# Kernel optimization log

Hardware: AMD Instinct MI355X
Metric: run time of the kernel (lower is better)

The kernel has to match this reference:

```python
import jax, jax.numpy as jnp
from jax import lax
import numpy as np

SAMPLE_RATIO = 0.25
K = 20          # nsample from group_args
SLOPE = 0.2     # leakyrelu negative_slope
EPS = 1e-5      # BatchNorm eps


def fps(p, m):
    """Furthest point sampling. p: [B,N,3] -> idx [B,m] int32."""
    B, N, _ = p.shape

    def step(carry, _):
        dist, last_idx = carry                      # [B,N], [B]
        last_pt = jnp.take_along_axis(p, last_idx[:, None, None], axis=1)  # [B,1,3]
        d = jnp.sum((p - last_pt) ** 2, axis=-1)    # [B,N]
        dist = jnp.minimum(dist, d)
        nxt = jnp.argmax(dist, axis=1).astype(jnp.int32)
        return (dist, nxt), last_idx

    dist0 = jnp.full((B, N), 1e10, dtype=p.dtype)
    idx0 = jnp.zeros((B,), dtype=jnp.int32)
    _, idxs = lax.scan(step, (dist0, idx0), None, length=m)
    return jnp.transpose(idxs)                      # [B,m]


def knn_idx(q, p, k):
    """q: [B,M,3] queries, p: [B,N,3] -> [B,M,k] indices of k nearest."""
    # squared distances, [B,M,N] (the memory-bound intermediate)
    d = (jnp.sum(q * q, -1)[:, :, None]
         + jnp.sum(p * p, -1)[:, None, :]
         - 2.0 * jnp.einsum('bmd,bnd->bmn', q, p))
    _, idx = lax.top_k(-d, k)
    return idx


def convblock(x, W, g, b):
    """1x1 Conv2d (bias=False) -> leakyrelu(0.2) -> BatchNorm2d (train-mode)."""
    x = jnp.einsum('oc,bcmk->bomk', W, x)
    x = jnp.where(x >= 0, x, SLOPE * x)
    mean = jnp.mean(x, axis=(0, 2, 3), keepdims=True)
    var = jnp.var(x, axis=(0, 2, 3), keepdims=True)
    return g[None, :, None, None] * (x - mean) * lax.rsqrt(var + EPS) + b[None, :, None, None]


def setup_inputs() -> dict:
    key = jax.random.key(0)
    ks = jax.random.split(key, 4)
    C = 64
    p = jax.random.normal(ks[0], (4, 8192, 3), dtype=jnp.float32)
    # kaiming-normal-ish conv weights (1x1 kernels flattened to [out,in])
    W1 = jax.random.normal(ks[1], (C, 6), dtype=jnp.float32) * np.sqrt(2.0 / 6)
    W2 = jax.random.normal(ks[2], (C, C), dtype=jnp.float32) * np.sqrt(2.0 / C)
    W3 = jax.random.normal(ks[3], (C, C), dtype=jnp.float32) * np.sqrt(2.0 / C)
    ones = jnp.ones((C,), jnp.float32)
    zeros = jnp.zeros((C,), jnp.float32)
    return {"p": p, "W1": W1, "g1": ones, "b1": zeros,
            "W2": W2, "g2": ones, "b2": zeros,
            "W3": W3, "g3": ones, "b3": zeros}


def reference(p, W1, g1, b1, W2, g2, b2, W3, g3, b3):
    B, N, _ = p.shape
    M = int(N * SAMPLE_RATIO)
    # features default to xyz: f = p^T, [B,3,N]; we keep [B,N,3] layout for gathers
    idx = fps(p, M)                                              # [B,M]
    p1 = jnp.take_along_axis(p, idx[:, :, None], axis=1)         # [B,M,3]
    nidx = knn_idx(p1, p, K)                                     # [B,M,K]
    batch = jnp.arange(B)[:, None, None]
    grouped = p[batch, nidx]                                     # [B,M,K,3] gathered xyz (== gathered features)
    dp = grouped - p1[:, :, None, :]                             # [B,M,K,3] relative coords
    # cat((dp, gf), dim=1) in channel-first layout -> [B,6,M,K]
    gf = jnp.concatenate([dp, grouped], axis=-1)                 # [B,M,K,6]
    x = jnp.transpose(gf, (0, 3, 1, 2))                          # [B,6,M,K]
    x = convblock(x, W1, g1, b1)
    x = convblock(x, W2, g2, b2)
    x = convblock(x, W3, g3, b3)
    return jnp.max(x, axis=-1)                                   # [B,64,M]
```

## Files before the change

### kernel.cpp

```cpp
#include <hip/hip_runtime.h>
#include <cstdint>
#include <cstddef>


#define B_ 4
#define N_ 8192
#define M_ 2048
#define K_ 20
#define BMK (B_*M_*K_)
#define EPS_ 1e-5f
#define TILE_ 1024
#define PERS 248

typedef unsigned long long ull;
typedef float f32x2 __attribute__((ext_vector_type(2)));

__device__ __forceinline__ ull packkey(float d, int idx) {
  unsigned int bb = __float_as_uint(d);
  bb ^= (bb & 0x80000000u) ? 0xFFFFFFFFu : 0x80000000u;
  return ((ull)bb << 32) | (unsigned int)idx;
}
__device__ __forceinline__ float keymaxf(ull k) {
  unsigned int hb = (unsigned int)(k >> 32);
  unsigned int fb = (hb & 0x80000000u) ? (hb ^ 0x80000000u) : ~hb;
  return __uint_as_float(fb);
}
__device__ __forceinline__ void insert20(ull* keys, ull key) {
#pragma unroll
  for (int i = 19; i > 0; --i) {
    ull lo = keys[i-1];
    keys[i] = (key < lo) ? lo : ((key < keys[i]) ? key : keys[i]);
  }
  keys[0] = (key < keys[0]) ? key : keys[0];
}

#define DPPMAXU(V, CTRL) {                                                           \
    unsigned int nh = (unsigned int)__builtin_amdgcn_update_dpp(                     \
        (int)V, (int)V, CTRL, 0xF, 0xF, false);                                      \
    V = (nh > V) ? nh : V; }

__global__ __launch_bounds__(512)
void fpsknn_kernel(const float* __restrict__ p, float* __restrict__ p1,
                   float* __restrict__ gfp, const float* __restrict__ W1,
                   float* __restrict__ stats, int* __restrict__ prog) {
  __shared__ union {
    struct { float4 pts4[N_]; unsigned int slotsv[2][8]; int idxsel[2]; } f;
    struct { float4 tile[TILE_]; ull mk[8*32*20]; float bs[128]; } k;
  } sm;
  const int tid = threadIdx.x;

  if (blockIdx.x < B_) {
#pragma clang fp contract(off)
    const int b = blockIdx.x;
    const float* pb = p + (size_t)b * (N_*3);
    float* p1b = p1 + (size_t)b * (M_*3);
    float4* pts4 = sm.f.pts4;
    const int wv = tid >> 6;
    const int base = tid * 16;
    f32x2 X[8], Y[8], Z[8], D[8];
#pragma unroll
    for (int j = 0; j < 8; ++j) {
      int i = base + 2*j;
      float x0 = pb[i*3+0], y0 = pb[i*3+1], z0 = pb[i*3+2];
      float x1 = pb[i*3+3], y1 = pb[i*3+4], z1 = pb[i*3+5];
      X[j] = (f32x2){x0, x1};
      Y[j] = (f32x2){y0, y1};
      Z[j] = (f32x2){z0, z1};
      D[j] = (f32x2){1e10f, 1e10f};
      pts4[i]   = make_float4(x0, y0, z0, 0.f);
      pts4[i+1] = make_float4(x1, y1, z1, 0.f);
    }
    if (tid < 2) sm.f.idxsel[tid] = 0x7FFFFFFF;
    float qx = pb[0], qy = pb[1], qz = pb[2];
    if (tid == 0) { p1b[0] = qx; p1b[1] = qy; p1b[2] = qz; }
    __syncthreads();
    for (int t = 1; t < M_; ++t) {
      const int cur = t & 1;
      f32x2 q2x = (f32x2){qx, qx};
      f32x2 q2y = (f32x2){qy, qy};
      f32x2 q2z = (f32x2){qz, qz};
      f32x2 tmx = (f32x2){-1.f, -1.f};
#pragma unroll
      for (int j = 0; j < 8; ++j) {
        f32x2 dx = X[j] - q2x;
        f32x2 dy = Y[j] - q2y;
        f32x2 dz = Z[j] - q2z;
        f32x2 s = (dx*dx + dy*dy) + dz*dz;
        f32x2 dj = __builtin_elementwise_min(D[j], s);
        D[j] = dj;
        tmx = __builtin_elementwise_max(tmx, dj);
      }
      float tm = fmaxf(tmx.x, tmx.y);
      const unsigned int tmb = __float_as_uint(tm);
      unsigned int hv = tmb;
      DPPMAXU(hv, 0x111)
      DPPMAXU(hv, 0x112)
      DPPMAXU(hv, 0x114)
      DPPMAXU(hv, 0x118)
      DPPMAXU(hv, 0x142)
      DPPMAXU(hv, 0x143)
      if ((tid & 63) == 63) sm.f.slotsv[cur][wv] = hv;
      __syncthreads();
      if (tid == 0) sm.f.idxsel[cur ^ 1] = 0x7FFFFFFF;
      unsigned int g = sm.f.slotsv[cur][0];
#pragma unroll
      for (int j = 1; j < 8; ++j) { unsigned int s2 = sm.f.slotsv[cur][j]; g = (s2 > g) ? s2 : g; }
      if (tmb == g) {
        int fj = 0x7FFFFFFF;
#pragma unroll
        for (int j = 7; j >= 0; --j) {
          if (__float_as_uint(D[j].y) == g) fj = base + 2*j + 1;
          if (__float_as_uint(D[j].x) == g) fj = base + 2*j;
        }
        atomicMin(&sm.f.idxsel[cur], fj);
      }
      __syncthreads();
      int sel = sm.f.idxsel[cur];
      sel = __builtin_amdgcn_readfirstlane(sel);
      float4 qv = pts4[sel];
      qx = qv.x; qy = qv.y; qz = qv.z;
      if (tid == 0) {
        p1b[t*3+0] = qx; p1b[t*3+1] = qy; p1b[t*3+2] = qz;
        if ((t & 63) == 63)
          __hip_atomic_store(&prog[b], t, __ATOMIC_RELEASE, __HIP_MEMORY_SCOPE_AGENT);
      }
    }
    if (tid == 0)
      __hip_atomic_store(&prog[b], M_, __ATOMIC_RELEASE, __HIP_MEMORY_SCOPE_AGENT);
    return;
  }

  float4* tile = sm.k.tile;
  ull* mk = sm.k.mk;
  float* gfl = (float*)sm.k.tile;
  float* bs = sm.k.bs;
  for (int ord = (int)blockIdx.x - B_; ord < 1024; ord += PERS) {
    const int b = ord & 3;
    const int q0 = (ord >> 2) * 8;
    if (tid == 0) {
      while (__hip_atomic_load(&prog[b], __ATOMIC_ACQUIRE, __HIP_MEMORY_SCOPE_AGENT) < q0 + 7)
        __builtin_amdgcn_s_sleep(16);
    }
    __syncthreads();
    { int pv = __hip_atomic_load(&prog[b], __ATOMIC_ACQUIRE, __HIP_MEMORY_SCOPE_AGENT);
      asm volatile("" :: "v"(pv)); }

    const int ql = (tid >> 5) & 7;
    const int part = tid & 31;
    const int m = q0 + ql;
    const float* pb = p + (size_t)b*(N_*3);
    const float* qp_ = p1 + ((size_t)b*M_ + m)*3;
    float qx = qp_[0], qy = qp_[1], qz = qp_[2];
    float qq = __fadd_rn(__fadd_rn(__fmul_rn(qx,qx), __fmul_rn(qy,qy)), __fmul_rn(qz,qz));
    ull keys[20];
#pragma unroll
    for (int i = 0; i < 20; ++i) keys[i] = 0xFF8000007FFFFFFFull;
    float maxf = __uint_as_float(0x7F800000u);
    for (int t0 = 0; t0 < N_; t0 += TILE_) {
      __syncthreads();
      for (int i = tid; i < TILE_; i += 512) {
        float x = pb[(t0+i)*3+0], y = pb[(t0+i)*3+1], z = pb[(t0+i)*3+2];
        float pp = __fadd_rn(__fadd_rn(__fmul_rn(x,x), __fmul_rn(y,y)), __fmul_rn(z,z));
        tile[i] = make_float4(x, y, z, pp);
      }
      __syncthreads();
      if (tid < 256) {
        const int sbase = part * 32;
        for (int s = 0; s < 32; ++s) {
          int ss = sbase + ((s + part) & 31);
          float4 pt = tile[ss];
          float qp = fmaf(pt.z, qz, fmaf(pt.y, qy, __fmul_rn(pt.x, qx)));
          float d = __fsub_rn(__fadd_rn(qq, pt.w), __fmul_rn(2.0f, qp));
          if (d <= maxf) {
            ull key = packkey(d, t0 + ss);
            if (key < keys[19]) { insert20(keys, key); maxf = keymaxf(keys[19]); }
          }
        }
      }
    }
    if (tid < 256) {
      ull* myslot = &mk[(ql*32 + part)*20];
#pragma unroll
      for (int i = 0; i < 20; ++i) myslot[i] = keys[i];
    }
    __syncthreads();
    if (tid < 256 && part == 0) {
      for (int pp2 = 1; pp2 < 32; ++pp2) {
        const ull* os = &mk[(ql*32 + pp2)*20];
        for (int i = 0; i < 20; ++i) {
          ull k = os[i];
          if (k >= keys[19]) break;
          insert20(keys, k);
        }
      }
      ull* myslot = &mk[(ql*32)*20];
#pragma unroll
      for (int i = 0; i < 20; ++i) myslot[i] = keys[i];
    }
    __syncthreads();
    for (int w = tid; w < 8*K_; w += 512) {
      int ql2 = w / K_;
      int kk = w - ql2*K_;
      ull key = mk[ql2*32*20 + kk];
      int idx = (int)(unsigned int)(key & 0xFFFFFFFFu);
      float gx = pb[idx*3+0], gy = pb[idx*3+1], gz = pb[idx*3+2];
      int m2 = q0 + ql2;
      const float* qv = p1 + ((size_t)b*M_ + m2)*3;
      size_t col = ((size_t)(b*M_ + m2))*K_ + kk;
      float d0 = __fsub_rn(gx, qv[0]);
      float d1 = __fsub_rn(gy, qv[1]);
      float d2 = __fsub_rn(gz, qv[2]);
      gfp[0*BMK + col] = d0;
      gfp[1*BMK + col] = d1;
      gfp[2*BMK + col] = d2;
      gfp[3*BMK + col] = gx;
      gfp[4*BMK + col] = gy;
      gfp[5*BMK + col] = gz;
      gfl[w*6+0] = d0; gfl[w*6+1] = d1; gfl[w*6+2] = d2;
      gfl[w*6+3] = gx; gfl[w*6+4] = gy; gfl[w*6+5] = gz;
    }
    __syncthreads();
    {
      const int lane = tid & 63;
      const int grp = tid >> 6;
      float w1r[6];
#pragma unroll
      for (int c = 0; c < 6; ++c) w1r[c] = W1[lane*6 + c];
      float acc = 0.f, accq = 0.f;
      for (int cc = 0; cc < 20; ++cc) {
        const float* gv = &gfl[(grp*20 + cc)*6];
        float y = __fmul_rn(w1r[0], gv[0]);
#pragma unroll
        for (int c = 1; c < 6; ++c) y = fmaf(w1r[c], gv[c], y);
        float u = (y >= 0.f) ? y : 0.2f*y;
        acc += u;
        accq = fmaf(u, u, accq);
      }
      if (tid < 128) bs[tid] = 0.f;
      __syncthreads();
      atomicAdd(&bs[lane], acc);
      atomicAdd(&bs[64+lane], accq);
      __syncthreads();
      if (tid < 128) atomicAdd(&stats[tid], bs[tid]);
    }
  }
}

__device__ __forceinline__ void bn_coeff(const float* __restrict__ st,
                                         const float* __restrict__ g,
                                         const float* __restrict__ bb,
                                         int o, float& A, float& C) {
  const float inv = 1.0f / (float)BMK;
  float mean = st[o] * inv;
  float var  = st[64+o] * inv - mean*mean;
  float a = g[o] / sqrtf(var + EPS_);
  A = a;
  C = fmaf(-a, mean, bb[o]);
}

__device__ __forceinline__ void gridbar(int* c, int expected) {
  __syncthreads();
  if (threadIdx.x == 0) {
    __hip_atomic_fetch_add(c, 1, __ATOMIC_ACQ_REL, __HIP_MEMORY_SCOPE_AGENT);
    while (__hip_atomic_load(c, __ATOMIC_ACQUIRE, __HIP_MEMORY_SCOPE_AGENT) < expected)
      __builtin_amdgcn_s_sleep(2);
  }
  __syncthreads();
}

__global__ __launch_bounds__(256)
void tail_kernel(const float* __restrict__ gfp, const float* __restrict__ W1,
                 float* __restrict__ stats,
                 const float* __restrict__ g1, const float* __restrict__ b1,
                 const float* __restrict__ W2, float* __restrict__ u2t,
                 const float* __restrict__ W3,
                 const float* __restrict__ g2, const float* __restrict__ b2,
                 const float* __restrict__ g3, const float* __restrict__ b3,
                 float* __restrict__ out, int* __restrict__ bar,
                 float* __restrict__ pmx, float* __restrict__ pmn) {
  const int tid = threadIdx.x;
  const int nblk = (int)gridDim.x;
  const int lane = tid & 63;
  const int wid = ((int)blockIdx.x*256 + tid) >> 6;
  const int nw = (nblk*256) >> 6;
  __shared__ float sA[64], sC[64];
  __shared__ float bs[128];
  __shared__ float xbuf[4][64];
  float* xb = xbuf[(tid >> 6) & 3];

  {
    if (tid < 64) bn_coeff(stats, g1, b1, tid, sA[tid], sC[tid]);
    __syncthreads();
    float w1r[6];
#pragma unroll
    for (int c = 0; c < 6; ++c) w1r[c] = W1[lane*6 + c];
    const float sAl = sA[lane], sCl = sC[lane];
    float wrow[64];
#pragma unroll
    for (int c = 0; c < 64; ++c) wrow[c] = W2[lane*64 + c];
    float acc = 0.f, accq = 0.f;
    float gfn[6];
    int col = wid;
    if (col < BMK) {
#pragma unroll
      for (int c = 0; c < 6; ++c) gfn[c] = gfp[c*BMK + col];
    }
    for (; col < BMK; col += nw) {
      float gfc[6];
#pragma unroll
      for (int c = 0; c < 6; ++c) gfc[c] = gfn[c];
      if (col + nw < BMK) {
#pragma unroll
        for (int c = 0; c < 6; ++c) gfn[c] = gfp[c*BMK + (col + nw)];
      }
      float y = __fmul_rn(w1r[0], gfc[0]);
#pragma unroll
      for (int c = 1; c < 6; ++c) y = fmaf(w1r[c], gfc[c], y);
      float u = (y >= 0.f) ? y : 0.2f*y;
      float x1v = fmaf(sAl, u, sCl);
      xb[lane] = x1v;
      float yo = 0.f;
      const float4* xb4 = (const float4*)xb;
#pragma unroll
      for (int c4 = 0; c4 < 16; ++c4) {
        float4 v = xb4[c4];
        yo = fmaf(wrow[4*c4+0], v.x, yo);
        yo = fmaf(wrow[4*c4+1], v.y, yo);
        yo = fmaf(wrow[4*c4+2], v.z, yo);
        yo = fmaf(wrow[4*c4+3], v.w, yo);
      }
      float u2 = (yo >= 0.f) ? yo : 0.2f*yo;
      u2t[(size_t)col*64 + lane] = u2;
      acc += u2;
      accq = fmaf(u2, u2, accq);
    }
    if (tid < 128) bs[tid] = 0.f;
    __syncthreads();
    atomicAdd(&bs[lane], acc);
    atomicAdd(&bs[64+lane], accq);
    __syncthreads();
    if (tid < 128) atomicAdd(&stats[128 + tid], bs[tid]);
  }
  gridbar(&bar[0], nblk);

  float w3[64];
  float bb = 0.f;
  {
    if (tid < 64) bn_coeff(stats + 128, g2, b2, tid, sA[tid], sC[tid]);
    __syncthreads();
#pragma unroll
    for (int c = 0; c < 64; ++c) w3[c] = W3[lane*64 + c] * sA[c];
#pragma unroll
    for (int c = 0; c < 64; ++c) bb = fmaf(W3[lane*64 + c], sC[c], bb);
    float acc = 0.f, accq = 0.f;
    for (int wv = wid; wv < B_*M_; wv += nw) {
      float mx = -3.4e38f, mn = 3.4e38f;
      for (int k = 0; k < K_; ++k) {
        const float4* u4 = (const float4*)(u2t + ((size_t)wv*K_ + k)*64);
        float y = bb;
#pragma unroll
        for (int c4 = 0; c4 < 16; ++c4) {
          float4 v = u4[c4];
          y = fmaf(w3[4*c4+0], v.x, y);
          y = fmaf(w3[4*c4+1], v.y, y);
          y = fmaf(w3[4*c4+2], v.z, y);
          y = fmaf(w3[4*c4+3], v.w, y);
        }
        float u = (y >= 0.f) ? y : 0.2f*y;
        acc += u; accq = fmaf(u, u, accq);
        mx = fmaxf(mx, u); mn = fminf(mn, u);
      }
      pmx[(size_t)wv*64 + lane] = mx;
      pmn[(size_t)wv*64 + lane] = mn;
    }
    if (tid < 128) bs[tid] = 0.f;
    __syncthreads();
    atomicAdd(&bs[lane], acc);
    atomicAdd(&bs[64+lane], accq);
    __syncthreads();
    if (tid < 128) atomicAdd(&stats[256 + tid], bs[tid]);
  }
  gridbar(&bar[1], nblk);

  {
    float A3, C3;
    bn_coeff(stats + 256, g3, b3, lane, A3, C3);
    for (int wv = wid; wv < B_*M_; wv += nw) {
      float mx = pmx[(size_t)wv*64 + lane];
      float mn = pmn[(size_t)wv*64 + lane];
      float r = (A3 >= 0.f) ? mx : mn;
      int b = wv >> 11, m = wv & 2047;
      out[((size_t)(b*64 + lane))*M_ + m] = fmaf(A3, r, C3);
    }
  }
}

extern "C" void kernel_launch(void* const* d_in, const int* in_sizes, int n_in,
                              void* d_out, int out_size, void* d_ws, size_t ws_size,
                              hipStream_t stream) {
  const float* p  = (const float*)d_in[0];
  const float* W1 = (const float*)d_in[1];
  const float* g1 = (const float*)d_in[2];
  const float* b1 = (const float*)d_in[3];
  const float* W2 = (const float*)d_in[4];
  const float* g2 = (const float*)d_in[5];
  const float* b2 = (const float*)d_in[6];
  const float* W3 = (const float*)d_in[7];
  const float* g3 = (const float*)d_in[8];
  const float* b3 = (const float*)d_in[9];
  float* out = (float*)d_out;
  char* ws = (char*)d_ws;

  float* p1    = (float*)(ws);
  float* gfp   = (float*)(ws + 131072);
  float* u2t   = (float*)(ws + 4194304);
  float* stats = (float*)(ws + 46137344);
  int*   prog  = (int*)(ws + 46138880);
  int*   bar   = (int*)(ws + 46138896);
  float* pmx   = (float*)(ws);
  float* pmn   = (float*)(ws + 2097152);

  hipMemsetAsync((void*)stats, 0, 1568, stream);
  hipLaunchKernelGGL(fpsknn_kernel, dim3(B_ + PERS), dim3(512), 0, stream,
                     p, p1, gfp, W1, stats, prog);
  hipLaunchKernelGGL(tail_kernel,   dim3(512), dim3(256), 0, stream,
                     gfp, W1, stats, g1, b1, W2, u2t, W3, g2, b2, g3, b3, out, bar,
                     pmx, pmn);
}
```

Before: 2.393 ms.

## Morton-sort points in FPS and skip distance updates via bounding-box pruning

Before furthest point sampling, each batch's points are bucketed into an 8x8x8 Morton grid and reordered so every thread holds a spatially compact set, with original indices kept for tie-breaking. Each iteration, a thread skips its distance updates when the lower bound from the new query to its bounding box exceeds its current max min-distance. This removes most per-iteration arithmetic on the serial FPS critical path. In exchange it adds a one-time sort with atomics and a prefix scan, and ties are broken by the packed original index to keep results exact.

New measurement: 2.284 ms, median of 2. 4.6% less time.

```diff
diff --git a/kernel.cpp b/kernel.cpp
--- a/kernel.cpp
+++ b/kernel.cpp
@@ -34,6 +34,18 @@
   keys[0] = (key < keys[0]) ? key : keys[0];
 }
 
+__device__ __forceinline__ unsigned int mapmono(float f) {
+  unsigned int u = __float_as_uint(f);
+  return u ^ ((u & 0x80000000u) ? 0xFFFFFFFFu : 0x80000000u);
+}
+__device__ __forceinline__ float unmapmono(unsigned int u) {
+  unsigned int f = (u & 0x80000000u) ? (u ^ 0x80000000u) : ~u;
+  return __uint_as_float(f);
+}
+__device__ __forceinline__ int mspread(int v) {
+  return (v & 1) | ((v & 2) << 2) | ((v & 4) << 4);
+}
+
 #define DPPMAXU(V, CTRL) {                                                           \
     unsigned int nh = (unsigned int)__builtin_amdgcn_update_dpp(                     \
         (int)V, (int)V, CTRL, 0xF, 0xF, false);                                      \
@@ -44,7 +56,8 @@
                    float* __restrict__ gfp, const float* __restrict__ W1,
                    float* __restrict__ stats, int* __restrict__ prog) {
   __shared__ union {
-    struct { float4 pts4[N_]; unsigned int slotsv[2][8]; int idxsel[2]; } f;
+    struct { float4 pts4[N_]; unsigned int slotsv[2][8]; int idxsel[2];
+             unsigned int hist[520]; } f;
     struct { float4 tile[TILE_]; ull mk[8*32*20]; float bs[128]; } k;
   } sm;
   const int tid = threadIdx.x;
@@ -55,43 +68,119 @@
     const float* pb = p + (size_t)b * (N_*3);
     float* p1b = p1 + (size_t)b * (M_*3);
     float4* pts4 = sm.f.pts4;
+    unsigned int* hist = sm.f.hist;
     const int wv = tid >> 6;
     const int base = tid * 16;
+
+    float tx[16], ty[16], tz[16];
+#pragma unroll
+    for (int j = 0; j < 16; ++j) {
+      int i = base + j;
+      tx[j] = pb[i*3+0]; ty[j] = pb[i*3+1]; tz[j] = pb[i*3+2];
+    }
+    for (int i = tid; i < 520; i += 512) hist[i] = 0;
+    __syncthreads();
+    {
+      unsigned int axp = 0, axn = 0, ayp = 0, ayn = 0, azp = 0, azn = 0;
+#pragma unroll
+      for (int j = 0; j < 16; ++j) {
+        axp = max(axp, mapmono(tx[j])); axn = max(axn, mapmono(-tx[j]));
+        ayp = max(ayp, mapmono(ty[j])); ayn = max(ayn, mapmono(-ty[j]));
+        azp = max(azp, mapmono(tz[j])); azn = max(azn, mapmono(-tz[j]));
+      }
+      atomicMax(&hist[512], axp); atomicMax(&hist[513], axn);
+      atomicMax(&hist[514], ayp); atomicMax(&hist[515], ayn);
+      atomicMax(&hist[516], azp); atomicMax(&hist[517], azn);
+    }
+    __syncthreads();
+    const float bminx = -unmapmono(hist[513]), bmaxx = unmapmono(hist[512]);
+    const float bminy = -unmapmono(hist[515]), bmaxy = unmapmono(hist[514]);
+    const float bminz = -unmapmono(hist[517]), bmaxz = unmapmono(hist[516]);
+    const float wx_ = bmaxx - bminx, wy_ = bmaxy - bminy, wz_ = bmaxz - bminz;
+    const float ivx = (wx_ > 0.f) ? 8.0f/wx_ : 0.f;
+    const float ivy = (wy_ > 0.f) ? 8.0f/wy_ : 0.f;
+    const float ivz = (wz_ > 0.f) ? 8.0f/wz_ : 0.f;
+    __syncthreads();
+#pragma unroll
+    for (int j = 0; j < 16; ++j) {
+      int kx = min((int)((tx[j]-bminx)*ivx), 7);
+      int ky = min((int)((ty[j]-bminy)*ivy), 7);
+      int kz = min((int)((tz[j]-bminz)*ivz), 7);
+      int cell = mspread(kx) | (mspread(ky) << 1) | (mspread(kz) << 2);
+      atomicAdd(&hist[cell], 1u);
+    }
+    __syncthreads();
+    {
+      unsigned int cnt = hist[tid];
+      unsigned int v = cnt;
+      for (int s = 1; s < 512; s <<= 1) {
+        unsigned int t2 = (tid >= s) ? hist[tid - s] : 0u;
+        __syncthreads();
+        v += t2;
+        hist[tid] = v;
+        __syncthreads();
+      }
+      hist[tid] = v - cnt;
+    }
+    __syncthreads();
+#pragma unroll
+    for (int j = 0; j < 16; ++j) {
+      int kx = min((int)((tx[j]-bminx)*ivx), 7);
+      int ky = min((int)((ty[j]-bminy)*ivy), 7);
+      int kz = min((int)((tz[j]-bminz)*ivz), 7);
+      int cell = mspread(kx) | (mspread(ky) << 1) | (mspread(kz) << 2);
+      unsigned int pos = atomicAdd(&hist[cell], 1u);
+      pts4[pos] = make_float4(tx[j], ty[j], tz[j], __int_as_float(base + j));
+    }
+    __syncthreads();
     f32x2 X[8], Y[8], Z[8], D[8];
+    int oidx[16];
+    float bxmn = 3.4e38f, bxmx = -3.4e38f, bymn = 3.4e38f, bymx = -3.4e38f;
+    float bzmn = 3.4e38f, bzmx = -3.4e38f;
 #pragma unroll
     for (int j = 0; j < 8; ++j) {
-      int i = base + 2*j;
-      float x0 = pb[i*3+0], y0 = pb[i*3+1], z0 = pb[i*3+2];
-      float x1 = pb[i*3+3], y1 = pb[i*3+4], z1 = pb[i*3+5];
-      X[j] = (f32x2){x0, x1};
-      Y[j] = (f32x2){y0, y1};
-      Z[j] = (f32x2){z0, z1};
+      float4 a = pts4[base + 2*j];
+      float4 c = pts4[base + 2*j + 1];
+      X[j] = (f32x2){a.x, c.x};
+      Y[j] = (f32x2){a.y, c.y};
+      Z[j] = (f32x2){a.z, c.z};
       D[j] = (f32x2){1e10f, 1e10f};
-      pts4[i]   = make_float4(x0, y0, z0, 0.f);
-      pts4[i+1] = make_float4(x1, y1, z1, 0.f);
-    }
+      oidx[2*j]   = __float_as_int(a.w);
+      oidx[2*j+1] = __float_as_int(c.w);
+      bxmn = fminf(bxmn, fminf(a.x, c.x)); bxmx = fmaxf(bxmx, fmaxf(a.x, c.x));
+      bymn = fminf(bymn, fminf(a.y, c.y)); bymx = fmaxf(bymx, fmaxf(a.y, c.y));
+      bzmn = fminf(bzmn, fminf(a.z, c.z)); bzmx = fmaxf(bzmx, fmaxf(a.z, c.z));
+    }
+    float cmax = 1e10f;
     if (tid < 2) sm.f.idxsel[tid] = 0x7FFFFFFF;
     float qx = pb[0], qy = pb[1], qz = pb[2];
     if (tid == 0) { p1b[0] = qx; p1b[1] = qy; p1b[2] = qz; }
     __syncthreads();
+
     for (int t = 1; t < M_; ++t) {
       const int cur = t & 1;
-      f32x2 q2x = (f32x2){qx, qx};
-      f32x2 q2y = (f32x2){qy, qy};
-      f32x2 q2z = (f32x2){qz, qz};
-      f32x2 tmx = (f32x2){-1.f, -1.f};
-#pragma unroll
-      for (int j = 0; j < 8; ++j) {
-        f32x2 dx = X[j] - q2x;
-        f32x2 dy = Y[j] - q2y;
-        f32x2 dz = Z[j] - q2z;
-        f32x2 s = (dx*dx + dy*dy) + dz*dz;
-        f32x2 dj = __builtin_elementwise_min(D[j], s);
-        D[j] = dj;
-        tmx = __builtin_elementwise_max(tmx, dj);
-      }
-      float tm = fmaxf(tmx.x, tmx.y);
-      const unsigned int tmb = __float_as_uint(tm);
+      float dxl = fmaxf(fmaxf(bxmn - qx, qx - bxmx), 0.f);
+      float dyl = fmaxf(fmaxf(bymn - qy, qy - bymx), 0.f);
+      float dzl = fmaxf(fmaxf(bzmn - qz, qz - bzmx), 0.f);
+      float slb = (dxl*dxl + dyl*dyl) + dzl*dzl;
+      if (slb <= cmax) {
+        f32x2 q2x = (f32x2){qx, qx};
+        f32x2 q2y = (f32x2){qy, qy};
+        f32x2 q2z = (f32x2){qz, qz};
+        f32x2 tmx = (f32x2){-1.f, -1.f};
+#pragma unroll
+        for (int j = 0; j < 8; ++j) {
+          f32x2 dx = X[j] - q2x;
+          f32x2 dy = Y[j] - q2y;
+          f32x2 dz = Z[j] - q2z;
+          f32x2 s = (dx*dx + dy*dy) + dz*dz;
+          f32x2 dj = __builtin_elementwise_min(D[j], s);
+          D[j] = dj;
+          tmx = __builtin_elementwise_max(tmx, dj);
+        }
+        cmax = fmaxf(tmx.x, tmx.y);
+      }
+      const unsigned int tmb = __float_as_uint(cmax);
       unsigned int hv = tmb;
       DPPMAXU(hv, 0x111)
       DPPMAXU(hv, 0x112)
@@ -106,18 +195,18 @@
 #pragma unroll
       for (int j = 1; j < 8; ++j) { unsigned int s2 = sm.f.slotsv[cur][j]; g = (s2 > g) ? s2 : g; }
       if (tmb == g) {
-        int fj = 0x7FFFFFFF;
-#pragma unroll
-        for (int j = 7; j >= 0; --j) {
-          if (__float_as_uint(D[j].y) == g) fj = base + 2*j + 1;
-          if (__float_as_uint(D[j].x) == g) fj = base + 2*j;
+        int best = 0x7FFFFFFF;
+#pragma unroll
+        for (int j = 0; j < 8; ++j) {
+          if (__float_as_uint(D[j].x) == g) best = min(best, (oidx[2*j]   << 13) | (base + 2*j));
+          if (__float_as_uint(D[j].y) == g) best = min(best, (oidx[2*j+1] << 13) | (base + 2*j + 1));
         }
-        atomicMin(&sm.f.idxsel[cur], fj);
+        atomicMin(&sm.f.idxsel[cur], best);
       }
       __syncthreads();
-      int sel = sm.f.idxsel[cur];
-      sel = __builtin_amdgcn_readfirstlane(sel);
-      float4 qv = pts4[sel];
+      int packed = sm.f.idxsel[cur];
+      packed = __builtin_amdgcn_readfirstlane(packed);
+      float4 qv = pts4[packed & 8191];
       qx = qv.x; qy = qv.y; qz = qv.z;
       if (tid == 0) {
         p1b[t*3+0] = qx; p1b[t*3+1] = qy; p1b[t*3+2] = qz;
```
